# Optimization experiments

Measured on AMD Instinct MI355X. Metric: run time of the kernel, lower is better.

Reference implementation:

```python
import jax, jax.numpy as jnp
import numpy as np

DIM = 1024
HEADS = 16
HEAD_DIM = DIM // HEADS
MLP_DIM = 4096
EPS = 1e-12  # F.normalize eps


def l2_rms(x, g):
    # repo RMSNorm: F.normalize(x, dim=-1) * sqrt(d) * g  (g is a scalar param)
    d = x.shape[-1]
    n = jnp.sqrt(jnp.sum(x * x, axis=-1, keepdims=True))
    return x / jnp.maximum(n, EPS) * (d ** 0.5) * g


def setup_inputs() -> dict:
    key = jax.random.key(0)
    ks = jax.random.split(key, 8)
    B, N = 2, 2048
    s = lambda fan_in: 1.0 / np.sqrt(fan_in)
    return {
        "x": jax.random.normal(ks[0], (B, N, DIM), jnp.float32),
        "w_qkv": jax.random.normal(ks[1], (DIM, 3 * DIM), jnp.float32) * s(DIM),
        "b_qkv": jnp.zeros((3 * DIM,), jnp.float32),
        "w_proj": jax.random.normal(ks[2], (DIM, DIM), jnp.float32) * s(DIM),
        "b_proj": jnp.zeros((DIM,), jnp.float32),
        "g_norm1": jnp.ones((1,), jnp.float32),
        "g_norm2": jnp.ones((1,), jnp.float32),
        "g_qnorm": jnp.ones((1,), jnp.float32),
        "g_knorm": jnp.ones((1,), jnp.float32),
        "w_fc1": jax.random.normal(ks[3], (DIM, MLP_DIM), jnp.float32) * s(DIM),
        "b_fc1": jnp.zeros((MLP_DIM,), jnp.float32),
        "w_fc2": jax.random.normal(ks[4], (MLP_DIM, DIM), jnp.float32) * s(MLP_DIM),
        "b_fc2": jnp.zeros((DIM,), jnp.float32),
    }


def reference(x, w_qkv, b_qkv, w_proj, b_proj, g_norm1, g_norm2,
              g_qnorm, g_knorm, w_fc1, b_fc1, w_fc2, b_fc2):
    B, N, D = x.shape
    # --- attention branch ---
    h = l2_rms(x, g_norm1)
    qkv = h @ w_qkv + b_qkv                      # [B,N,3D]
    qkv = qkv.reshape(B, N, 3, HEADS, HEAD_DIM)
    q, k, v = [jnp.transpose(qkv[:, :, i], (0, 2, 1, 3)) for i in range(3)]  # [B,H,N,d]
    q = l2_rms(q, g_qnorm)
    k = l2_rms(k, g_knorm)
    scale = HEAD_DIM ** -0.5
    scores = jnp.einsum('bhqd,bhkd->bhqk', q * scale, k)   # explicit [B,H,N,N]
    attn = jax.nn.softmax(scores, axis=-1)
    o = jnp.einsum('bhqk,bhkd->bhqd', attn, v)
    o = jnp.transpose(o, (0, 2, 1, 3)).reshape(B, N, D)
    x = x + (o @ w_proj + b_proj)
    # --- MLP branch ---
    h = l2_rms(x, g_norm2)
    h = jax.nn.gelu(h @ w_fc1 + b_fc1, approximate=True)
    x = x + (h @ w_fc2 + b_fc2)
    return x
```

## Files before the change

kernel.cpp:

```cpp
#include <hip/hip_runtime.h>
#include <stdint.h>

#define SEQ_ 2048
#define DIM_ 1024
#define HD_ 64
#define NH_ 16

typedef __bf16 bf16x8 __attribute__((ext_vector_type(8)));
typedef float f32x4 __attribute__((ext_vector_type(4)));
typedef __attribute__((address_space(1))) unsigned int as1_uint;
typedef __attribute__((address_space(3))) unsigned int as3_uint;

__device__ __forceinline__ unsigned short f2bf(float f) {
  unsigned u = __builtin_bit_cast(unsigned, f);
  u += 0x7fffu + ((u >> 16) & 1u);
  return (unsigned short)(u >> 16);
}

__device__ __forceinline__ void gload_lds16(const void* g, void* l) {
  __builtin_amdgcn_global_load_lds(
      reinterpret_cast<as1_uint*>(reinterpret_cast<uintptr_t>(g)),
      reinterpret_cast<as3_uint*>(
          static_cast<unsigned int>(reinterpret_cast<uintptr_t>(l))),
      16, 0, 0);
}

__global__ __launch_bounds__(256) void transpose_cvt(
    const float* __restrict__ W, unsigned short* __restrict__ Wt, int K, int N) {
  __shared__ float t[32][33];
  const int tx = threadIdx.x & 31, ty = threadIdx.x >> 5;
  const int n0 = blockIdx.x * 32, k0 = blockIdx.y * 32;
#pragma unroll
  for (int i = 0; i < 4; i++)
    t[ty + i * 8][tx] = W[(size_t)(k0 + ty + i * 8) * N + n0 + tx];
  __syncthreads();
#pragma unroll
  for (int i = 0; i < 4; i++)
    Wt[(size_t)(n0 + ty + i * 8) * K + k0 + tx] = f2bf(t[tx][ty + i * 8]);
}

__global__ __launch_bounds__(256) void rmsnorm_k(
    const float* __restrict__ x, const float* __restrict__ g,
    unsigned short* __restrict__ out) {
  const int row = blockIdx.x;
  const float4* xr = (const float4*)(x + (size_t)row * DIM_);
  float4 v = xr[threadIdx.x];
  float ss = v.x * v.x + v.y * v.y + v.z * v.z + v.w * v.w;
  ss += __shfl_xor(ss, 1);  ss += __shfl_xor(ss, 2);  ss += __shfl_xor(ss, 4);
  ss += __shfl_xor(ss, 8);  ss += __shfl_xor(ss, 16); ss += __shfl_xor(ss, 32);
  __shared__ float red[4];
  if ((threadIdx.x & 63) == 0) red[threadIdx.x >> 6] = ss;
  __syncthreads();
  float tot = red[0] + red[1] + red[2] + red[3];
  float sc = 32.0f * g[0] / fmaxf(sqrtf(tot), 1e-12f);
  unsigned short* orow = out + (size_t)row * DIM_;
  const int b4 = threadIdx.x * 4;
  orow[b4 + 0] = f2bf(v.x * sc);
  orow[b4 + 1] = f2bf(v.y * sc);
  orow[b4 + 2] = f2bf(v.z * sc);
  orow[b4 + 3] = f2bf(v.w * sc);
}

template <int EPI>
__global__ __launch_bounds__(256, 2) void gemm_bf16(
    const unsigned short* __restrict__ A, const unsigned short* __restrict__ Bt,
    const float* __restrict__ bias, const float* __restrict__ res,
    void* __restrict__ Cout, int M, int N, int K) {
  __shared__ __align__(16) unsigned short As[128 * 32];
  __shared__ __align__(16) unsigned short Bs[128 * 32];
  const int tid = threadIdx.x;
  const int w = tid >> 6, lane = tid & 63;
  const int wm = w >> 1, wn = w & 1;
  const int quad = lane >> 4, l15 = lane & 15;
  const int bn = blockIdx.x, bm = blockIdx.y;

  f32x4 acc[4][4];
#pragma unroll
  for (int i = 0; i < 4; i++)
#pragma unroll
    for (int j = 0; j < 4; j++) acc[i][j] = f32x4{0.f, 0.f, 0.f, 0.f};

  const int r0 = w * 16 + (lane >> 2);
  const int c0 = (lane & 3) * 8;
  const unsigned short* gA0 = A + (size_t)(bm * 128 + r0) * K + c0;
  const unsigned short* gA1 = gA0 + (size_t)64 * K;
  const unsigned short* gB0 = Bt + (size_t)(bn * 128 + r0) * K + c0;
  const unsigned short* gB1 = gB0 + (size_t)64 * K;
  unsigned short* lA0 = As + w * 512;
  unsigned short* lA1 = As + 2048 + w * 512;
  unsigned short* lB0 = Bs + w * 512;
  unsigned short* lB1 = Bs + 2048 + w * 512;

  for (int kk = 0; kk < K; kk += 32) {
    gload_lds16(gA0, lA0);
    gload_lds16(gA1, lA1);
    gload_lds16(gB0, lB0);
    gload_lds16(gB1, lB1);
    gA0 += 32; gA1 += 32; gB0 += 32; gB1 += 32;
    __syncthreads();
    bf16x8 af[4], bf[4];
#pragma unroll
    for (int i = 0; i < 4; i++) {
      af[i] = *(const bf16x8*)&As[(wm * 64 + i * 16 + l15) * 32 + quad * 8];
      bf[i] = *(const bf16x8*)&Bs[(wn * 64 + i * 16 + l15) * 32 + quad * 8];
    }
#pragma unroll
    for (int i = 0; i < 4; i++)
#pragma unroll
      for (int j = 0; j < 4; j++)
        acc[i][j] = __builtin_amdgcn_mfma_f32_16x16x32_bf16(af[i], bf[j], acc[i][j], 0, 0, 0);
    __syncthreads();
  }

  const int rowb = bm * 128 + wm * 64;
  const int colb = bn * 128 + wn * 64;
#pragma unroll
  for (int i = 0; i < 4; i++) {
#pragma unroll
    for (int j = 0; j < 4; j++) {
      const int col = colb + j * 16 + l15;
      const float bv = bias[col];
#pragma unroll
      for (int r = 0; r < 4; r++) {
        const int row = rowb + i * 16 + quad * 4 + r;
        const size_t idx = (size_t)row * N + col;
        float v = acc[i][j][r] + bv;
        if (EPI == 0) {
          ((float*)Cout)[idx] = v;
        } else if (EPI == 1) {
          ((float*)Cout)[idx] = v + res[idx];
        } else {
          float t = tanhf(0.7978845608028654f * (v + 0.044715f * v * v * v));
          ((unsigned short*)Cout)[idx] = f2bf(0.5f * v * (1.0f + t));
        }
      }
    }
  }
}

__global__ __launch_bounds__(256) void qkv_post(
    const float* __restrict__ qkv, const float* __restrict__ gq,
    const float* __restrict__ gk, unsigned short* __restrict__ Qs,
    unsigned short* __restrict__ Ks, unsigned short* __restrict__ VT) {
  const int item = blockIdx.x * 4 + (threadIdx.x >> 6);
  const int lane = threadIdx.x & 63;
  const int h = item & 15;
  const int rn = item >> 4;
  const int b = rn >> 11, n = rn & 2047;
  const float* base = qkv + (size_t)rn * 3072 + h * 64;
  const float qv = base[lane];
  const float kv = base[1024 + lane];
  const float vv = base[2048 + lane];
  float sq = qv * qv, sk = kv * kv;
  sq += __shfl_xor(sq, 1);  sk += __shfl_xor(sk, 1);
  sq += __shfl_xor(sq, 2);  sk += __shfl_xor(sk, 2);
  sq += __shfl_xor(sq, 4);  sk += __shfl_xor(sk, 4);
  sq += __shfl_xor(sq, 8);  sk += __shfl_xor(sk, 8);
  sq += __shfl_xor(sq, 16); sk += __shfl_xor(sk, 16);
  sq += __shfl_xor(sq, 32); sk += __shfl_xor(sk, 32);
  const float qs = qv / fmaxf(sqrtf(sq), 1e-12f) * gq[0];
  const float ks = kv / fmaxf(sqrtf(sk), 1e-12f) * (8.0f * gk[0]);
  const int bh = b * 16 + h;
  Qs[((size_t)bh * SEQ_ + n) * HD_ + lane] = f2bf(qs);
  Ks[((size_t)bh * SEQ_ + n) * HD_ + lane] = f2bf(ks);
  VT[((size_t)bh * HD_ + lane) * SEQ_ + n] = f2bf(vv);
}

#define PLD_ 72
__global__ __launch_bounds__(256) void attn_fwd(
    const unsigned short* __restrict__ Qs, const unsigned short* __restrict__ Ks,
    const unsigned short* __restrict__ VT, const float* __restrict__ gq,
    const float* __restrict__ gk, unsigned short* __restrict__ O) {
  __shared__ __align__(16) unsigned short Kl[2][64][32];
  __shared__ __align__(16) unsigned short Vl[2][64][32];
  __shared__ __align__(16) unsigned short Pl[4][16 * PLD_];
  const int bh = blockIdx.x, qt = blockIdx.y;
  const int w = threadIdx.x >> 6, lane = threadIdx.x & 63;
  const int quad = lane >> 4, l15 = lane & 15;
  const float M = 8.0f * fabsf(gq[0] * gk[0]);
  const unsigned short* Qb = Qs + (size_t)bh * SEQ_ * HD_;
  const unsigned short* Kb = Ks + (size_t)bh * SEQ_ * HD_;
  const unsigned short* Vb = VT + (size_t)bh * HD_ * SEQ_;
  const int q0 = qt * 64 + w * 16;
  const bf16x8 qa0 = *(const bf16x8*)&Qb[(q0 + l15) * HD_ + quad * 8];
  const bf16x8 qa1 = *(const bf16x8*)&Qb[(q0 + l15) * HD_ + 32 + quad * 8];

  const unsigned short* gsrc[4];
  unsigned short* ldst[4];
  int gstep[4];
#pragma unroll
  for (int i = 0; i < 4; i++) {
    const int idx = w * 4 + i;
    if (idx < 8) {
      const int kc = idx >> 2, kh = idx & 3;
      ldst[i] = &Kl[kc][kh * 16][0];
      gsrc[i] = &Kb[(size_t)(kh * 16 + (lane >> 2)) * HD_ + kc * 32 + (lane & 3) * 8];
      gstep[i] = 64 * HD_;
    } else {
      const int j = idx - 8;
      const int kc = j >> 2, dh = j & 3;
      ldst[i] = &Vl[kc][dh * 16][0];
      gsrc[i] = &Vb[(size_t)(dh * 16 + (lane >> 2)) * SEQ_ + kc * 32 + (lane & 3) * 8];
      gstep[i] = 64;
    }
  }

  f32x4 o[4];
  float lsum[4] = {0.f, 0.f, 0.f, 0.f};
#pragma unroll
  for (int c = 0; c < 4; c++) o[c] = f32x4{0.f, 0.f, 0.f, 0.f};
  unsigned short* Pw = &Pl[w][0];

  for (int kt = 0; kt < SEQ_ / 64; kt++) {
#pragma unroll
    for (int i = 0; i < 4; i++) {
      gload_lds16(gsrc[i], ldst[i]);
      gsrc[i] += gstep[i];
    }
    __syncthreads();
    f32x4 s[4];
#pragma unroll
    for (int kn = 0; kn < 4; kn++) {
      const bf16x8 kf0 = *(const bf16x8*)&Kl[0][kn * 16 + l15][quad * 8];
      const bf16x8 kf1 = *(const bf16x8*)&Kl[1][kn * 16 + l15][quad * 8];
      s[kn] = __builtin_amdgcn_mfma_f32_16x16x32_bf16(qa0, kf0, f32x4{0.f, 0.f, 0.f, 0.f}, 0, 0, 0);
      s[kn] = __builtin_amdgcn_mfma_f32_16x16x32_bf16(qa1, kf1, s[kn], 0, 0, 0);
    }
#pragma unroll
    for (int kn = 0; kn < 4; kn++)
#pragma unroll
      for (int r = 0; r < 4; r++) {
        const float p = __expf(s[kn][r] - M);
        lsum[r] += p;
        Pw[(quad * 4 + r) * PLD_ + kn * 16 + l15] = f2bf(p);
      }
    asm volatile("s_waitcnt lgkmcnt(0)" ::: "memory");
    const bf16x8 pa0 = *(const bf16x8*)&Pw[l15 * PLD_ + quad * 8];
    const bf16x8 pa1 = *(const bf16x8*)&Pw[l15 * PLD_ + 32 + quad * 8];
#pragma unroll
    for (int c = 0; c < 4; c++) {
      const bf16x8 vf0 = *(const bf16x8*)&Vl[0][c * 16 + l15][quad * 8];
      const bf16x8 vf1 = *(const bf16x8*)&Vl[1][c * 16 + l15][quad * 8];
      o[c] = __builtin_amdgcn_mfma_f32_16x16x32_bf16(pa0, vf0, o[c], 0, 0, 0);
      o[c] = __builtin_amdgcn_mfma_f32_16x16x32_bf16(pa1, vf1, o[c], 0, 0, 0);
    }
    __syncthreads();
  }

#pragma unroll
  for (int r = 0; r < 4; r++) {
    lsum[r] += __shfl_xor(lsum[r], 1);
    lsum[r] += __shfl_xor(lsum[r], 2);
    lsum[r] += __shfl_xor(lsum[r], 4);
    lsum[r] += __shfl_xor(lsum[r], 8);
    lsum[r] = 1.0f / lsum[r];
  }
  const int b = bh >> 4, h = bh & 15;
#pragma unroll
  for (int c = 0; c < 4; c++)
#pragma unroll
    for (int r = 0; r < 4; r++) {
      const int row = q0 + quad * 4 + r;
      O[((size_t)(b * SEQ_ + row)) * DIM_ + h * 64 + c * 16 + l15] =
          f2bf(o[c][r] * lsum[r]);
    }
}

extern "C" void kernel_launch(void* const* d_in, const int* in_sizes, int n_in,
                              void* d_out, int out_size, void* d_ws, size_t ws_size,
                              hipStream_t stream) {
  const float* x      = (const float*)d_in[0];
  const float* w_qkv  = (const float*)d_in[1];
  const float* b_qkv  = (const float*)d_in[2];
  const float* w_proj = (const float*)d_in[3];
  const float* b_proj = (const float*)d_in[4];
  const float* g1     = (const float*)d_in[5];
  const float* g2     = (const float*)d_in[6];
  const float* gq     = (const float*)d_in[7];
  const float* gk     = (const float*)d_in[8];
  const float* w_fc1  = (const float*)d_in[9];
  const float* b_fc1  = (const float*)d_in[10];
  const float* w_fc2  = (const float*)d_in[11];
  const float* b_fc2  = (const float*)d_in[12];
  float* out = (float*)d_out;

  char* p = (char*)d_ws;
  auto alloc = [&](size_t bytes) {
    char* r = p;
    p += (bytes + 255) & ~(size_t)255;
    return r;
  };
  unsigned short* wqkvT  = (unsigned short*)alloc(3072ull * 1024 * 2);
  unsigned short* wprojT = (unsigned short*)alloc(1024ull * 1024 * 2);
  unsigned short* wfc1T  = (unsigned short*)alloc(4096ull * 1024 * 2);
  unsigned short* wfc2T  = (unsigned short*)alloc(1024ull * 4096 * 2);
  unsigned short* h1     = (unsigned short*)alloc(4096ull * 1024 * 2);
  char* big = alloc(4096ull * 3072 * 4);
  float* qkvf = (float*)big;
  unsigned short* h3 = (unsigned short*)big;
  unsigned short* QsB = (unsigned short*)alloc(32ull * SEQ_ * HD_ * 2);
  unsigned short* KsB = (unsigned short*)alloc(32ull * SEQ_ * HD_ * 2);
  unsigned short* VTB = (unsigned short*)alloc(32ull * SEQ_ * HD_ * 2);
  float* x2 = (float*)alloc(4096ull * 1024 * 4);
  unsigned short* h2 = (unsigned short*)alloc(4096ull * 1024 * 2);
  unsigned short* Obuf = h1;

  transpose_cvt<<<dim3(3072 / 32, 1024 / 32), 256, 0, stream>>>(w_qkv, wqkvT, 1024, 3072);
  transpose_cvt<<<dim3(1024 / 32, 1024 / 32), 256, 0, stream>>>(w_proj, wprojT, 1024, 1024);
  transpose_cvt<<<dim3(4096 / 32, 1024 / 32), 256, 0, stream>>>(w_fc1, wfc1T, 1024, 4096);
  transpose_cvt<<<dim3(1024 / 32, 4096 / 32), 256, 0, stream>>>(w_fc2, wfc2T, 4096, 1024);
  rmsnorm_k<<<4096, 256, 0, stream>>>(x, g1, h1);
  gemm_bf16<0><<<dim3(3072 / 128, 4096 / 128), 256, 0, stream>>>(
      h1, wqkvT, b_qkv, nullptr, qkvf, 4096, 3072, 1024);
  qkv_post<<<16384, 256, 0, stream>>>(qkvf, gq, gk, QsB, KsB, VTB);
  attn_fwd<<<dim3(32, 32), 256, 0, stream>>>(QsB, KsB, VTB, gq, gk, Obuf);
  gemm_bf16<1><<<dim3(1024 / 128, 4096 / 128), 256, 0, stream>>>(
      Obuf, wprojT, b_proj, x, x2, 4096, 1024, 1024);
  rmsnorm_k<<<4096, 256, 0, stream>>>(x2, g2, h2);
  gemm_bf16<2><<<dim3(4096 / 128, 4096 / 128), 256, 0, stream>>>(
      h2, wfc1T, b_fc1, nullptr, h3, 4096, 4096, 1024);
  gemm_bf16<1><<<dim3(1024 / 128, 4096 / 128), 256, 0, stream>>>(
      h3, wfc2T, b_fc2, x2, out, 4096, 1024, 4096);
}
```

Measured before the change: 428.7 us.

## Add split-K with reduction for output GEMMs and emit bf16 QKV

The proj and fc2 GEMMs launch only 256 tiles each. When the workspace is large enough, they are now split along K across gridDim.z. Each slice writes fp32 partials, and a separate reduce kernel adds the partials, bias and residual. The QKV GEMM now stores bf16 instead of fp32, roughly halving its write traffic and the reads in qkv_post. The cost is extra partial-buffer traffic plus one more launch per split GEMM, and a small precision loss in the stored QKV values. Split-K only runs if the remaining workspace clears the 64MB/96MB thresholds.

```diff
diff --git a/kernel.cpp b/kernel.cpp
--- a/kernel.cpp
+++ b/kernel.cpp
@@ -15,6 +15,9 @@
   unsigned u = __builtin_bit_cast(unsigned, f);
   u += 0x7fffu + ((u >> 16) & 1u);
   return (unsigned short)(u >> 16);
+}
+__device__ __forceinline__ float bf2f(unsigned short u) {
+  return __builtin_bit_cast(float, ((unsigned)u) << 16);
 }
 
 __device__ __forceinline__ void gload_lds16(const void* g, void* l) {
@@ -73,6 +76,8 @@
   const int wm = w >> 1, wn = w & 1;
   const int quad = lane >> 4, l15 = lane & 15;
   const int bn = blockIdx.x, bm = blockIdx.y;
+  const int Kchunk = K / gridDim.z;
+  const int kbeg = blockIdx.z * Kchunk;
 
   f32x4 acc[4][4];
 #pragma unroll
@@ -82,16 +87,16 @@
 
   const int r0 = w * 16 + (lane >> 2);
   const int c0 = (lane & 3) * 8;
-  const unsigned short* gA0 = A + (size_t)(bm * 128 + r0) * K + c0;
+  const unsigned short* gA0 = A + (size_t)(bm * 128 + r0) * K + kbeg + c0;
   const unsigned short* gA1 = gA0 + (size_t)64 * K;
-  const unsigned short* gB0 = Bt + (size_t)(bn * 128 + r0) * K + c0;
+  const unsigned short* gB0 = Bt + (size_t)(bn * 128 + r0) * K + kbeg + c0;
   const unsigned short* gB1 = gB0 + (size_t)64 * K;
   unsigned short* lA0 = As + w * 512;
   unsigned short* lA1 = As + 2048 + w * 512;
   unsigned short* lB0 = Bs + w * 512;
   unsigned short* lB1 = Bs + 2048 + w * 512;
 
-  for (int kk = 0; kk < K; kk += 32) {
+  for (int kk = 0; kk < Kchunk; kk += 32) {
     gload_lds16(gA0, lA0);
     gload_lds16(gA1, lA1);
     gload_lds16(gB0, lB0);
@@ -114,32 +119,51 @@
 
   const int rowb = bm * 128 + wm * 64;
   const int colb = bn * 128 + wn * 64;
+  float* Cz = (float*)Cout + (size_t)blockIdx.z * M * N;
 #pragma unroll
   for (int i = 0; i < 4; i++) {
 #pragma unroll
     for (int j = 0; j < 4; j++) {
       const int col = colb + j * 16 + l15;
-      const float bv = bias[col];
+      const float bv = (EPI == 3) ? 0.0f : bias[col];
 #pragma unroll
       for (int r = 0; r < 4; r++) {
         const int row = rowb + i * 16 + quad * 4 + r;
         const size_t idx = (size_t)row * N + col;
         float v = acc[i][j][r] + bv;
         if (EPI == 0) {
-          ((float*)Cout)[idx] = v;
+          ((unsigned short*)Cout)[idx] = f2bf(v);
         } else if (EPI == 1) {
           ((float*)Cout)[idx] = v + res[idx];
-        } else {
+        } else if (EPI == 2) {
           float t = tanhf(0.7978845608028654f * (v + 0.044715f * v * v * v));
           ((unsigned short*)Cout)[idx] = f2bf(0.5f * v * (1.0f + t));
+        } else {
+          Cz[idx] = v;
         }
       }
     }
   }
 }
 
+__global__ __launch_bounds__(256) void reduce_splitk(
+    const float* __restrict__ part, int S, const float* __restrict__ res,
+    const float* __restrict__ bias, float* __restrict__ out, int N, size_t MN) {
+  const size_t n4 = MN >> 2;
+  const size_t i = (size_t)blockIdx.x * 256 + threadIdx.x;
+  if (i >= n4) return;
+  float4 a = ((const float4*)res)[i];
+  float4 b = ((const float4*)bias)[i % (size_t)(N >> 2)];
+  float sx = a.x + b.x, sy = a.y + b.y, sz = a.z + b.z, sw = a.w + b.w;
+  for (int z = 0; z < S; z++) {
+    float4 p = ((const float4*)part)[z * n4 + i];
+    sx += p.x; sy += p.y; sz += p.z; sw += p.w;
+  }
+  ((float4*)out)[i] = make_float4(sx, sy, sz, sw);
+}
+
 __global__ __launch_bounds__(256) void qkv_post(
-    const float* __restrict__ qkv, const float* __restrict__ gq,
+    const unsigned short* __restrict__ qkv, const float* __restrict__ gq,
     const float* __restrict__ gk, unsigned short* __restrict__ Qs,
     unsigned short* __restrict__ Ks, unsigned short* __restrict__ VT) {
   const int item = blockIdx.x * 4 + (threadIdx.x >> 6);
@@ -147,10 +171,10 @@
   const int h = item & 15;
   const int rn = item >> 4;
   const int b = rn >> 11, n = rn & 2047;
-  const float* base = qkv + (size_t)rn * 3072 + h * 64;
-  const float qv = base[lane];
-  const float kv = base[1024 + lane];
-  const float vv = base[2048 + lane];
+  const unsigned short* base = qkv + (size_t)rn * 3072 + h * 64;
+  const float qv = bf2f(base[lane]);
+  const float kv = bf2f(base[1024 + lane]);
+  const float vv = bf2f(base[2048 + lane]);
   float sq = qv * qv, sk = kv * kv;
   sq += __shfl_xor(sq, 1);  sk += __shfl_xor(sk, 1);
   sq += __shfl_xor(sq, 2);  sk += __shfl_xor(sk, 2);
@@ -290,20 +314,27 @@
     p += (bytes + 255) & ~(size_t)255;
     return r;
   };
+  const size_t MB = 1ull << 20;
   unsigned short* wqkvT  = (unsigned short*)alloc(3072ull * 1024 * 2);
   unsigned short* wprojT = (unsigned short*)alloc(1024ull * 1024 * 2);
   unsigned short* wfc1T  = (unsigned short*)alloc(4096ull * 1024 * 2);
   unsigned short* wfc2T  = (unsigned short*)alloc(1024ull * 4096 * 2);
   unsigned short* h1     = (unsigned short*)alloc(4096ull * 1024 * 2);
-  char* big = alloc(4096ull * 3072 * 4);
-  float* qkvf = (float*)big;
-  unsigned short* h3 = (unsigned short*)big;
   unsigned short* QsB = (unsigned short*)alloc(32ull * SEQ_ * HD_ * 2);
   unsigned short* KsB = (unsigned short*)alloc(32ull * SEQ_ * HD_ * 2);
   unsigned short* VTB = (unsigned short*)alloc(32ull * SEQ_ * HD_ * 2);
   float* x2 = (float*)alloc(4096ull * 1024 * 4);
   unsigned short* h2 = (unsigned short*)alloc(4096ull * 1024 * 2);
+  char* big = p;
+  const size_t rem = ws_size - (size_t)(p - (char*)d_ws);
+  unsigned short* qkvb = (unsigned short*)big;
+  unsigned short* h3   = (unsigned short*)big;
+  float* proj_part = (float*)big;
+  float* fc2_part  = (float*)(big + 32 * MB);
+  const int S_pr  = rem >= 64 * MB ? 2 : 1;
+  const int S_fc2 = rem >= 96 * MB ? 4 : (rem >= 64 * MB ? 2 : 1);
   unsigned short* Obuf = h1;
+  const size_t MN = 4096ull * 1024;
 
   transpose_cvt<<<dim3(3072 / 32, 1024 / 32), 256, 0, stream>>>(w_qkv, wqkvT, 1024, 3072);
   transpose_cvt<<<dim3(1024 / 32, 1024 / 32), 256, 0, stream>>>(w_proj, wprojT, 1024, 1024);
@@ -311,14 +342,28 @@
   transpose_cvt<<<dim3(1024 / 32, 4096 / 32), 256, 0, stream>>>(w_fc2, wfc2T, 4096, 1024);
   rmsnorm_k<<<4096, 256, 0, stream>>>(x, g1, h1);
   gemm_bf16<0><<<dim3(3072 / 128, 4096 / 128), 256, 0, stream>>>(
-      h1, wqkvT, b_qkv, nullptr, qkvf, 4096, 3072, 1024);
-  qkv_post<<<16384, 256, 0, stream>>>(qkvf, gq, gk, QsB, KsB, VTB);
+      h1, wqkvT, b_qkv, nullptr, qkvb, 4096, 3072, 1024);
+  qkv_post<<<16384, 256, 0, stream>>>(qkvb, gq, gk, QsB, KsB, VTB);
   attn_fwd<<<dim3(32, 32), 256, 0, stream>>>(QsB, KsB, VTB, gq, gk, Obuf);
-  gemm_bf16<1><<<dim3(1024 / 128, 4096 / 128), 256, 0, stream>>>(
-      Obuf, wprojT, b_proj, x, x2, 4096, 1024, 1024);
+  if (S_pr > 1) {
+    gemm_bf16<3><<<dim3(1024 / 128, 4096 / 128, S_pr), 256, 0, stream>>>(
+        Obuf, wprojT, b_proj, nullptr, proj_part, 4096, 1024, 1024);
+    reduce_splitk<<<(MN / 4 + 255) / 256, 256, 0, stream>>>(
+        proj_part, S_pr, x, b_proj, x2, 1024, MN);
+  } else {
+    gemm_bf16<1><<<dim3(1024 / 128, 4096 / 128), 256, 0, stream>>>(
+        Obuf, wprojT, b_proj, x, x2, 4096, 1024, 1024);
+  }
   rmsnorm_k<<<4096, 256, 0, stream>>>(x2, g2, h2);
   gemm_bf16<2><<<dim3(4096 / 128, 4096 / 128), 256, 0, stream>>>(
       h2, wfc1T, b_fc1, nullptr, h3, 4096, 4096, 1024);
-  gemm_bf16<1><<<dim3(1024 / 128, 4096 / 128), 256, 0, stream>>>(
-      h3, wfc2T, b_fc2, x2, out, 4096, 1024, 4096);
-}
+  if (S_fc2 > 1) {
+    gemm_bf16<3><<<dim3(1024 / 128, 4096 / 128, S_fc2), 256, 0, stream>>>(
+        h3, wfc2T, b_fc2, nullptr, fc2_part, 4096, 1024, 4096);
+    reduce_splitk<<<(MN / 4 + 255) / 256, 256, 0, stream>>>(
+        fc2_part, S_fc2, x2, b_fc2, out, 1024, MN);
+  } else {
+    gemm_bf16<1><<<dim3(1024 / 128, 4096 / 128), 256, 0, stream>>>(
+        h3, wfc2T, b_fc2, x2, out, 4096, 1024, 4096);
+  }
+}
```

New measurement: 426.5 us. No clear change (-0.5%).
